# Optimization experiments

Hardware: AMD Instinct MI355X
Metric: run time of the kernel (lower is better)

Reference implementation:

```python
import jax, jax.numpy as jnp
import numpy as np

B, TC, TT, E, V = 512, 64, 16, 512, 256
E2 = E // 2


def entmax15(z):
    # exact sort-based 1.5-entmax over last axis (Peters et al., 2019)
    z = z / 2.0
    z = z - jnp.max(z, axis=-1, keepdims=True)  # shift-invariant, for stability
    z_srt = -jnp.sort(-z, axis=-1)
    d = z.shape[-1]
    rho = jnp.arange(1, d + 1, dtype=z.dtype)
    mean = jnp.cumsum(z_srt, axis=-1) / rho
    mean_sq = jnp.cumsum(z_srt * z_srt, axis=-1) / rho
    ss = rho * (mean_sq - mean * mean)
    delta = (1.0 - ss) / rho
    pos = delta > 0
    sqrt_d = jnp.where(pos, jnp.sqrt(jnp.where(pos, delta, 1.0)), 0.0)
    tau = mean - sqrt_d
    k = jnp.sum((tau <= z_srt).astype(jnp.int32), axis=-1, keepdims=True)
    tau_star = jnp.take_along_axis(tau, k - 1, axis=-1)
    y = jnp.clip(z - tau_star, 0.0)
    return y * y


def _mha(q_seq, kv, wq, wk, wv, bq, bk, bv, wo, bo):
    # single-head attention; q_seq: (T,B,E) decoder states, kv: (B,S,E) encoder memory
    e = q_seq.shape[-1]
    q = (q_seq @ wq.T + bq) * (1.0 / jnp.sqrt(jnp.asarray(e, q_seq.dtype)))
    k = kv @ wk.T + bk
    v = kv @ wv.T + bv
    a = jax.nn.softmax(jnp.einsum('tbe,bse->bts', q, k), axis=-1)
    o = jnp.einsum('bts,bse->tbe', a, v)
    return o @ wo.T + bo


def setup_inputs() -> dict:
    key = jax.random.key(0)
    ks = jax.random.split(key, 20)
    rn = lambda k, s, sc=1.0: sc * jax.random.normal(k, s, dtype=jnp.float32)
    z = lambda s: jnp.zeros(s, jnp.float32)
    return {
        'char_encoding': rn(ks[0], (B, TC, E)),
        'char_hn0': rn(ks[1], (B, E2)),
        'char_cn0': rn(ks[2], (B, E2)),
        'tag_encoding': rn(ks[3], (B, TT, E)),
        'tag_hn0': rn(ks[4], (B, E2)),
        'tag_cn0': rn(ks[5], (B, E2)),
        'true_output_seq': jax.random.uniform(ks[6], (B, TC, V), dtype=jnp.float32),
        'w_ih': rn(ks[7], (4 * E, V), 0.05),
        'w_hh': rn(ks[8], (4 * E, E), 0.05),
        'b_ih': z((4 * E,)),
        'b_hh': z((4 * E,)),
        'char_wq': rn(ks[9], (E, E), 0.05), 'char_wk': rn(ks[10], (E, E), 0.05), 'char_wv': rn(ks[11], (E, E), 0.05),
        'char_bq': z((E,)), 'char_bk': z((E,)), 'char_bv': z((E,)),
        'char_wo': rn(ks[12], (E, E), 0.05), 'char_bo': z((E,)),
        'tag_wq': rn(ks[13], (E, E), 0.05), 'tag_wk': rn(ks[14], (E, E), 0.05), 'tag_wv': rn(ks[15], (E, E), 0.05),
        'tag_bq': z((E,)), 'tag_bk': z((E,)), 'tag_bv': z((E,)),
        'tag_wo': rn(ks[16], (E, E), 0.05), 'tag_bo': z((E,)),
        'out_w': rn(ks[17], (V, 2 * E), 0.05),
        'out_b': z((V,)),
    }


def reference(char_encoding, char_hn0, char_cn0, tag_encoding, tag_hn0, tag_cn0, true_output_seq, w_ih, w_hh, b_ih, b_hh, char_wq, char_wk, char_wv, char_bq, char_bk, char_bv, char_wo, char_bo, tag_wq, tag_wk, tag_wv, tag_bq, tag_bk, tag_bv, tag_wo, tag_bo, out_w, out_b):
    # initial cell state = concat of the two encoders' final (h, c)
    h0 = jnp.concatenate([char_hn0, tag_hn0], axis=-1)
    c0 = jnp.concatenate([char_cn0, tag_cn0], axis=-1)
    # teacher forcing: input at t=0 is zeros, then true_output_seq[:, t]
    xs = jnp.concatenate([jnp.zeros_like(true_output_seq[:, :1]), true_output_seq[:, 1:]], axis=1)
    xs = jnp.swapaxes(xs, 0, 1)  # (T, B, V)

    def cell(carry, x):
        h, c = carry
        gates = x @ w_ih.T + b_ih + h @ w_hh.T + b_hh
        i, f, g, o = jnp.split(gates, 4, axis=-1)  # torch gate order i,f,g,o
        c = jax.nn.sigmoid(f) * c + jax.nn.sigmoid(i) * jnp.tanh(g)
        h = jax.nn.sigmoid(o) * jnp.tanh(c)
        return (h, c), h

    _, hs = jax.lax.scan(cell, (h0, c0), xs)  # (T, B, E)
    # attention queries only depend on per-step h, so batch all T queries at once
    ca = _mha(hs, char_encoding, char_wq, char_wk, char_wv, char_bq, char_bk, char_bv, char_wo, char_bo)
    ta = _mha(hs, tag_encoding, tag_wq, tag_wk, tag_wv, tag_bq, tag_bk, tag_bv, tag_wo, tag_bo)
    logits = jnp.concatenate([ca, ta], axis=-1) @ out_w.T + out_b  # (T, B, V)
    return jnp.swapaxes(entmax15(logits), 0, 1)  # (B, T, V)
```

## Files before the change

### kernel.cpp

```cpp
#include <hip/hip_runtime.h>

typedef unsigned short us;
typedef unsigned int u32;
typedef unsigned long long u64;
typedef __bf16 bf16x8 __attribute__((ext_vector_type(8)));
typedef float f32x4 __attribute__((ext_vector_type(4)));

#define MFMA(a,b,c) __builtin_amdgcn_mfma_f32_16x16x32_bf16(a,b,c,0,0,0)

__device__ __forceinline__ us f2bf(float f){
  u32 u = __builtin_bit_cast(u32, f);
  u += 0x7fffu + ((u>>16)&1u);
  return (us)(u>>16);
}
__device__ __forceinline__ float bf2f(us h){
  u32 u = ((u32)h)<<16;
  return __builtin_bit_cast(float, u);
}
__device__ __forceinline__ float sigf(float x){ return 1.0f/(1.0f+__expf(-x)); }
__device__ __forceinline__ float tanh_(float x){ float e=__expf(2.0f*x); return 1.0f - 2.0f/(e+1.0f); }


__global__ void k_prep_wperm(const float* __restrict__ w_hh, const float* __restrict__ w_ih,
                             const float* __restrict__ b_ih, const float* __restrict__ b_hh,
                             us* __restrict__ Wp, float* __restrict__ biasc){
  int n = blockIdx.x; int c = threadIdx.x;
  float v = (c < 512) ? w_hh[(size_t)n*512 + c] : w_ih[(size_t)n*256 + (c-512)];
  int g = n >> 9, eg = n & 511, eb = eg >> 4, ln = eg & 15;
  int kc = c >> 5, qd = (c >> 3) & 3, i = c & 7;
  size_t dst = ((((size_t)eb*24 + kc)*4 + g)*64 + (size_t)(qd*16 + ln))*8 + i;
  Wp[dst] = f2bf(v);
  if (c == 0) biasc[n] = b_ih[n] + b_hh[n];
}

__global__ void k_prep_state(const float* __restrict__ ch, const float* __restrict__ th,
                             const float* __restrict__ cc, const float* __restrict__ tc,
                             us* __restrict__ h0, float* __restrict__ c0){
  int i = blockIdx.x*256 + threadIdx.x;
  int b = i>>9, e = i&511;
  float hv = (e<256)? ch[b*256+e] : th[b*256+e-256];
  float cv = (e<256)? cc[b*256+e] : tc[b*256+e-256];
  h0[i] = f2bf(hv); c0[i] = cv;
}

__global__ void k_xprep(const float* __restrict__ x, us* __restrict__ xbf){
  int g = blockIdx.x*256 + threadIdx.x;
  int v0 = (g & 31) * 8;
  int b  = (g >> 5) & 511;
  int t  = g >> 14;
  const float4* src = (const float4*)(x + ((size_t)(b*64 + t))*256 + v0);
  float4 f0 = src[0], f1 = src[1];
  uint4 pk;
  pk.x = (u32)f2bf(f0.x) | ((u32)f2bf(f0.y)<<16);
  pk.y = (u32)f2bf(f0.z) | ((u32)f2bf(f0.w)<<16);
  pk.z = (u32)f2bf(f1.x) | ((u32)f2bf(f1.y)<<16);
  pk.w = (u32)f2bf(f1.z) | ((u32)f2bf(f1.w)<<16);
  *(uint4*)(xbf + ((size_t)t*512 + b)*256 + v0) = pk;
}

__global__ void k_uvec(const float* __restrict__ bq, const float* __restrict__ wk,
                       float* __restrict__ u){
  int j = blockIdx.x*128 + threadIdx.x;
  float a = 0.f;
  for (int e=0;e<512;++e) a += bq[e]*wk[(size_t)e*512 + j];
  u[j] = a;
}

__global__ void k_pvec(const float* __restrict__ wo, const float* __restrict__ bv,
                       const float* __restrict__ bo, float* __restrict__ p){
  int i = blockIdx.x*128 + threadIdx.x;
  float a = bo[i];
  for (int j=0;j<512;++j) a += wo[(size_t)i*512+j]*bv[j];
  p[i] = a;
}

__global__ void k_bc(const float* __restrict__ out_w, const float* __restrict__ pc,
                     const float* __restrict__ pt, const float* __restrict__ out_b,
                     float* __restrict__ bc){
  int v = threadIdx.x;
  float a = out_b[v];
  for (int i=0;i<512;++i) a += out_w[(size_t)v*1024+i]*pc[i];
  for (int i=0;i<512;++i) a += out_w[(size_t)v*1024+512+i]*pt[i];
  bc[v] = a;
}

template<bool TA, int OMODE>
__global__ __launch_bounds__(256) void k_pgemm(const float* __restrict__ A, int lda,
    const float* __restrict__ B, int ldb, void* C1, void* C2, int ldc, int K){
  __shared__ us As[64][40];
  __shared__ us Bs[64][40];
  int tid=threadIdx.x, w=tid>>6, lane=tid&63, qd=lane>>4, ln=lane&15;
  int m0 = blockIdx.x*64, n0 = blockIdx.y*64;
  f32x4 acc[4] = {};
  for (int kc=0; kc<K/32; ++kc){
    int k0 = kc*32;
    if (!TA){
      int r=tid>>2, c=(tid&3)*8;
      const float* ap = A + (size_t)(m0+r)*lda + k0 + c;
      float4 f0=*(const float4*)ap, f1=*(const float4*)(ap+4);
      uint4 pk;
      pk.x=(u32)f2bf(f0.x)|((u32)f2bf(f0.y)<<16);
      pk.y=(u32)f2bf(f0.z)|((u32)f2bf(f0.w)<<16);
      pk.z=(u32)f2bf(f1.x)|((u32)f2bf(f1.y)<<16);
      pk.w=(u32)f2bf(f1.z)|((u32)f2bf(f1.w)<<16);
      *(uint4*)&As[r][c] = pk;
    } else {
      int kk=tid>>3, mp=(tid&7)*8;
      const float* ap = A + (size_t)(k0+kk)*lda + m0 + mp;
      #pragma unroll
      for (int i=0;i<8;++i) As[mp+i][kk] = f2bf(ap[i]);
    }
    { int kk=tid>>3, np=(tid&7)*8;
      const float* bp = B + (size_t)(k0+kk)*ldb + n0 + np;
      #pragma unroll
      for (int i=0;i<8;++i) Bs[np+i][kk] = f2bf(bp[i]);
    }
    __syncthreads();
    bf16x8 a = *(const bf16x8*)&As[16*w+ln][qd*8];
    #pragma unroll
    for (int j=0;j<4;++j){
      bf16x8 bb = *(const bf16x8*)&Bs[16*j+ln][qd*8];
      acc[j] = MFMA(a, bb, acc[j]);
    }
    __syncthreads();
  }
  #pragma unroll
  for (int j=0;j<4;++j){
    #pragma unroll
    for (int r=0;r<4;++r){
      size_t idx = (size_t)(m0+16*w+qd*4+r)*ldc + (n0+16*j+ln);
      float v = acc[j][r];
      if (OMODE==0) ((float*)C1)[idx] = v;
      else if (OMODE==1) ((us*)C1)[idx] = f2bf(v);
      else {
        us h = f2bf(v);
        ((us*)C1)[idx] = h;
        ((us*)C2)[idx] = f2bf(v - bf2f(h));
      }
    }
  }
}

__global__ __launch_bounds__(256, 1) void k_lstm_all(
    const us* __restrict__ h0, const us* __restrict__ xbf,
    const us* __restrict__ Wp, const float* __restrict__ biasc,
    const float* __restrict__ c0, us* __restrict__ hs,
    unsigned* __restrict__ bars){
  extern __shared__ us Wf[];
  int tid = threadIdx.x, w = tid>>6, lane = tid&63, qd = lane>>4, ln = lane&15;
  int bb = blockIdx.x & 7, eb = blockIdx.x >> 3;
  int b0 = bb*64, e0 = eb*16;
  {
    const uint4* src = (const uint4*)(Wp + (size_t)eb*49152);
    uint4* dst = (uint4*)Wf;
    #pragma unroll
    for (int i=0;i<24;++i) dst[tid + 256*i] = src[tid + 256*i];
  }
  int bA = b0 + 16*w + ln;
  int bC = b0 + 16*w + qd*4;
  int e  = e0 + ln;
  float bias_[4], c_[4];
  #pragma unroll
  for (int j=0;j<4;++j) bias_[j] = biasc[j*512 + e];
  #pragma unroll
  for (int r=0;r<4;++r) c_[r] = c0[(size_t)(bC+r)*512 + e];
  __syncthreads();
  unsigned* bar = bars + bb*64;
  f32x4 xacc[4] = {};
  for (int t=0; t<64; ++t){
    if (t > 0){
      unsigned tgt = 32u*(unsigned)t;
      while (__hip_atomic_load(bar, __ATOMIC_RELAXED, __HIP_MEMORY_SCOPE_AGENT) < tgt)
        __builtin_amdgcn_s_sleep(1);
    }
    bf16x8 afr[16];
    if (t == 0){
      const us* hrow = h0 + (size_t)bA*512;
      #pragma unroll
      for (int kc=0; kc<16; ++kc)
        afr[kc] = *(const bf16x8*)(hrow + kc*32 + qd*8);
    } else {
      const u64* hq = (const u64*)(hs + ((size_t)bA*64 + (t-1))*512);
      u64 q0[16], q1[16];
      #pragma unroll
      for (int kc=0; kc<16; ++kc){
        q0[kc] = __hip_atomic_load(hq + kc*8 + qd*2 + 0, __ATOMIC_RELAXED, __HIP_MEMORY_SCOPE_AGENT);
        q1[kc] = __hip_atomic_load(hq + kc*8 + qd*2 + 1, __ATOMIC_RELAXED, __HIP_MEMORY_SCOPE_AGENT);
      }
      #pragma unroll
      for (int kc=0; kc<16; ++kc){
        union { u64 q[2]; bf16x8 v; } u_;
        u_.q[0] = q0[kc]; u_.q[1] = q1[kc];
        afr[kc] = u_.v;
      }
    }
    f32x4 acc[4] = {xacc[0], xacc[1], xacc[2], xacc[3]};
    #pragma unroll
    for (int kc=0; kc<16; ++kc){
      #pragma unroll
      for (int j=0;j<4;++j){
        bf16x8 bfrag = *(const bf16x8*)&Wf[(size_t)((kc*4+j)*64 + lane)*8];
        acc[j] = MFMA(afr[kc], bfrag, acc[j]);
      }
    }
    us hb[4];
    #pragma unroll
    for (int r=0;r<4;++r){
      float iv = acc[0][r]+bias_[0], fv = acc[1][r]+bias_[1];
      float gv = acc[2][r]+bias_[2], ov = acc[3][r]+bias_[3];
      float cc2 = sigf(fv)*c_[r] + sigf(iv)*tanh_(gv);
      c_[r] = cc2;
      hb[r] = f2bf(sigf(ov)*tanh_(cc2));
    }
    #pragma unroll
    for (int r=0;r<4;++r){
      u32 v = hb[r];
      u32 p = v | (((u32)__shfl_xor((int)v, 1)) << 16);
      u64 q = (u64)p | (((u64)(u32)__shfl_xor((int)p, 2)) << 32);
      if ((lane & 3) == 0){
        size_t idx = ((size_t)(bC+r)*64 + t)*512 + e0 + ln;
        __hip_atomic_store((u64*)(hs + idx), q, __ATOMIC_RELAXED, __HIP_MEMORY_SCOPE_AGENT);
      }
    }
    if (t < 63){
      __syncthreads();
      if (tid == 0)
        __hip_atomic_fetch_add(bar, 1u, __ATOMIC_RELAXED, __HIP_MEMORY_SCOPE_AGENT);
      const us* xrow = xbf + ((size_t)(t+1)*512 + bA)*256;
      f32x4 xa[4] = {};
      #pragma unroll
      for (int kx=0; kx<8; ++kx){
        bf16x8 xf = *(const bf16x8*)(xrow + kx*32 + qd*8);
        #pragma unroll
        for (int j=0;j<4;++j){
          bf16x8 bfrag = *(const bf16x8*)&Wf[(size_t)(((16+kx)*4+j)*64 + lane)*8];
          xa[j] = MFMA(xf, bfrag, xa[j]);
        }
      }
      #pragma unroll
      for (int j=0;j<4;++j) xacc[j] = xa[j];
    }
  }
}

__global__ __launch_bounds__(256) void k_gemm(
    const us* __restrict__ Ap, const us* __restrict__ W,
    const float* __restrict__ bias, float alpha, us* __restrict__ C){
  __shared__ us As[128][40];
  __shared__ us Ws[128][40];
  int tid = threadIdx.x; int w = tid>>6; int lane=tid&63;
  int qd=lane>>4, ln=lane&15;
  int m0 = blockIdx.x*128, n0 = blockIdx.y*128;
  int wm = (w&1)*64, wn=(w>>1)*64;
  f32x4 acc[4][4] = {};
  int row = tid>>1; int cp = (tid&1)*16;
  for (int kc=0;kc<16;++kc){
    int k0=kc*32;
    { const uint4* ap = (const uint4*)(Ap + (size_t)(m0+row)*512 + k0+cp);
      *(uint4*)&As[row][cp]=ap[0]; *(uint4*)&As[row][cp+8]=ap[1];
    }
    { const uint4* wp = (const uint4*)(W + (size_t)(n0+row)*512 + k0+cp);
      *(uint4*)&Ws[row][cp]=wp[0]; *(uint4*)&Ws[row][cp+8]=wp[1];
    }
    __syncthreads();
    bf16x8 af[4], bfr[4];
    #pragma unroll
    for (int i=0;i<4;++i) af[i]  = *(const bf16x8*)&As[wm+16*i+ln][qd*8];
    #pragma unroll
    for (int j=0;j<4;++j) bfr[j] = *(const bf16x8*)&Ws[wn+16*j+ln][qd*8];
    #pragma unroll
    for (int i=0;i<4;++i)
      #pragma unroll
      for (int j=0;j<4;++j) acc[i][j]=MFMA(af[i],bfr[j],acc[i][j]);
    __syncthreads();
  }
  #pragma unroll
  for (int j=0;j<4;++j){
    int col = n0+wn+16*j+ln;
    float bv = bias[col];
    #pragma unroll
    for (int i=0;i<4;++i){
      #pragma unroll
      for (int r=0;r<4;++r){
        int rm = m0+wm+16*i+qd*4+r;
        C[(size_t)rm*512 + col] = f2bf(alpha*(acc[i][j][r]+bv));
      }
    }
  }
}

template<int S>
struct alignas(16) ASmem3 {
  static constexpr int SP  = (S<32)?32:S;
  static constexpr int SPp = SP+8;
  us Pbh[64][SPp];
  us Pbl[64][SPp];
  union {
    us Es[S][72];
    struct { us Eh[64][72]; us El[64][72]; } t;
  } u;
  us Ph[64][72];
  us Pl[64][72];
};

template<int S, bool ACC>
__global__ __launch_bounds__(256) void k_attn3(const us* __restrict__ hGp,
    const float* __restrict__ enc, const us* __restrict__ Mvh,
    const us* __restrict__ Mvl, float* __restrict__ out){
  constexpr int NJ  = S/16;
  constexpr int KC2 = ((S<32)?32:S)/32;
  extern __shared__ char smraw[];
  ASmem3<S>& sm = *reinterpret_cast<ASmem3<S>*>(smraw);
  int b = blockIdx.x;
  int tid=threadIdx.x, w=tid>>6, lane=tid&63, qd=lane>>4, ln=lane&15;

  f32x4 sacc[NJ];
  #pragma unroll
  for (int j=0;j<NJ;++j) sacc[j] = (f32x4){0.f,0.f,0.f,0.f};
  const us* hrow = hGp + ((size_t)(b*64 + 16*w + ln))*512;
  for (int ec=0; ec<8; ++ec){
    int e0 = ec*64;
    { int s = tid>>2, ep=(tid&3)*16;
      if (S==64 || tid < 4*S){
        const float* ap = enc + ((size_t)b*S + s)*512 + e0 + ep;
        float4 f0=*(const float4*)ap, f1=*(const float4*)(ap+4);
        float4 f2=*(const float4*)(ap+8), f3=*(const float4*)(ap+12);
        float fv[16]={f0.x,f0.y,f0.z,f0.w,f1.x,f1.y,f1.z,f1.w,
                      f2.x,f2.y,f2.z,f2.w,f3.x,f3.y,f3.z,f3.w};
        u32 pk[8];
        #pragma unroll
        for (int i=0;i<8;++i)
          pk[i] = (u32)f2bf(fv[2*i]) | ((u32)f2bf(fv[2*i+1])<<16);
        uint4* d = (uint4*)&sm.u.Es[s][ep];
        d[0] = make_uint4(pk[0],pk[1],pk[2],pk[3]);
        d[1] = make_uint4(pk[4],pk[5],pk[6],pk[7]);
      }
    }
    __syncthreads();
    #pragma unroll
    for (int kcl=0;kcl<2;++kcl){
      bf16x8 a = *(const bf16x8*)(hrow + e0 + kcl*32 + qd*8);
      #pragma unroll
      for (int j=0;j<NJ;++j){
        bf16x8 bb = *(const bf16x8*)&sm.u.Es[16*j+ln][kcl*32+qd*8];
        sacc[j] = MFMA(a, bb, sacc[j]);
      }
    }
    __syncthreads();
  }

  #pragma unroll
  for (int r=0;r<4;++r){
    float m = sacc[0][r];
    #pragma unroll
    for (int j=1;j<NJ;++j) m = fmaxf(m, sacc[j][r]);
    #pragma unroll
    for (int dl=1; dl<16; dl<<=1) m = fmaxf(m, __shfl_xor(m, dl));
    float ssum = 0.f;
    #pragma unroll
    for (int j=0;j<NJ;++j){ float e_=__expf(sacc[j][r]-m); sacc[j][r]=e_; ssum+=e_; }
    #pragma unroll
    for (int dl=1; dl<16; dl<<=1) ssum += __shfl_xor(ssum, dl);
    float inv = 1.0f/ssum;
    int R = 16*w + qd*4 + r;
    #pragma unroll
    for (int j=0;j<NJ;++j){
      float pv = sacc[j][r]*inv;
      us h = f2bf(pv);
      sm.Pbh[R][16*j+ln] = h;
      sm.Pbl[R][16*j+ln] = f2bf(pv - bf2f(h));
    }
    if (S==16){ sm.Pbh[R][16+ln]=0; sm.Pbl[R][16+ln]=0; }
  }

  f32x4 Lacc[4][4] = {};
  for (int ec=0; ec<8; ++ec){
    int e0 = ec*64;
    { int s = tid>>2, ep=(tid&3)*16;
      if (S==64 || tid < 4*S){
        const float* ap = enc + ((size_t)b*S + s)*512 + e0 + ep;
        float4 f0=*(const float4*)ap, f1=*(const float4*)(ap+4);
        float4 f2=*(const float4*)(ap+8), f3=*(const float4*)(ap+12);
        float fv[16]={f0.x,f0.y,f0.z,f0.w,f1.x,f1.y,f1.z,f1.w,
                      f2.x,f2.y,f2.z,f2.w,f3.x,f3.y,f3.z,f3.w};
        #pragma unroll
        for (int i=0;i<16;++i){
          float v = fv[i]; us h = f2bf(v);
          sm.u.t.Eh[ep+i][s] = h;
          sm.u.t.El[ep+i][s] = f2bf(v - bf2f(h));
        }
      } else if (S==16 && tid < 128){
        int s2 = 16 + ((tid-64)>>2);
        #pragma unroll
        for (int i=0;i<16;++i){ sm.u.t.Eh[ep+i][s2]=0; sm.u.t.El[ep+i][s2]=0; }
      }
    }
    __syncthreads();
    f32x4 pacc[4] = {};
    #pragma unroll
    for (int kcl=0;kcl<KC2;++kcl){
      bf16x8 ah = *(const bf16x8*)&sm.Pbh[16*w+ln][kcl*32+qd*8];
      bf16x8 al = *(const bf16x8*)&sm.Pbl[16*w+ln][kcl*32+qd*8];
      #pragma unroll
      for (int j=0;j<4;++j){
        bf16x8 bh = *(const bf16x8*)&sm.u.t.Eh[16*j+ln][kcl*32+qd*8];
        bf16x8 bl = *(const bf16x8*)&sm.u.t.El[16*j+ln][kcl*32+qd*8];
        pacc[j] = MFMA(ah, bh, pacc[j]);
        pacc[j] = MFMA(ah, bl, pacc[j]);
        pacc[j] = MFMA(al, bh, pacc[j]);
      }
    }
    #pragma unroll
    for (int j=0;j<4;++j)
      #pragma unroll
      for (int r=0;r<4;++r){
        float v = pacc[j][r]; us h = f2bf(v);
        sm.Ph[16*w+qd*4+r][16*j+ln] = h;
        sm.Pl[16*w+qd*4+r][16*j+ln] = f2bf(v - bf2f(h));
      }
    __syncthreads();
    #pragma unroll
    for (int kcl=0;kcl<2;++kcl){
      bf16x8 ah[4], al[4];
      #pragma unroll
      for (int i=0;i<4;++i){
        ah[i] = *(const bf16x8*)&sm.Ph[16*i+ln][kcl*32+qd*8];
        al[i] = *(const bf16x8*)&sm.Pl[16*i+ln][kcl*32+qd*8];
      }
      #pragma unroll
      for (int j=0;j<4;++j){
        int v = 64*w + 16*j + ln;
        bf16x8 mh = *(const bf16x8*)(Mvh + (size_t)v*512 + e0 + kcl*32 + qd*8);
        bf16x8 ml = *(const bf16x8*)(Mvl + (size_t)v*512 + e0 + kcl*32 + qd*8);
        #pragma unroll
        for (int i=0;i<4;++i){
          Lacc[i][j] = MFMA(ah[i], mh, Lacc[i][j]);
          Lacc[i][j] = MFMA(ah[i], ml, Lacc[i][j]);
          Lacc[i][j] = MFMA(al[i], mh, Lacc[i][j]);
        }
      }
    }
  }
  #pragma unroll
  for (int i=0;i<4;++i){
    #pragma unroll
    for (int j=0;j<4;++j){
      int v = 64*w + 16*j + ln;
      #pragma unroll
      for (int r=0;r<4;++r){
        size_t addr = ((size_t)b*64 + 16*i + qd*4 + r)*256 + v;
        if (ACC) out[addr] += Lacc[i][j][r];
        else     out[addr]  = Lacc[i][j][r];
      }
    }
  }
}

__global__ __launch_bounds__(256) void k_entmax(float* __restrict__ out,
                                                const float* __restrict__ bc){
  int tid=threadIdx.x; int w=tid>>6; int lane=tid&63;
  float4 bcv = *(const float4*)(bc + lane*4);
  int base = blockIdx.x*16 + w*4;
  for (int i=0;i<4;++i){
    int row = base + i;
    float* rp = out + (size_t)row*256 + lane*4;
    float4 d = *(const float4*)rp;
    float z[4] = {0.5f*(d.x+bcv.x), 0.5f*(d.y+bcv.y), 0.5f*(d.z+bcv.z), 0.5f*(d.w+bcv.w)};
    float m = fmaxf(fmaxf(z[0],z[1]), fmaxf(z[2],z[3]));
    #pragma unroll
    for (int dl=1; dl<64; dl<<=1) m = fmaxf(m, __shfl_xor(m, dl));
    #pragma unroll
    for (int k=0;k<4;++k) z[k] -= m;
    float tau = -1.0f;
    for (int it=0; it<14; ++it){
      float s1=0.f, s2=0.f;
      #pragma unroll
      for (int k=0;k<4;++k){
        float dd = z[k]-tau; dd = fmaxf(dd, 0.f);
        s1 += dd; s2 += dd*dd;
      }
      #pragma unroll
      for (int dl=1; dl<64; dl<<=1){ s1 += __shfl_xor(s1, dl); s2 += __shfl_xor(s2, dl); }
      tau += (s2 - 1.0f) / (2.0f*fmaxf(s1, 1e-12f));
    }
    float4 y;
    { float dd;
      dd = fmaxf(z[0]-tau,0.f); y.x = dd*dd;
      dd = fmaxf(z[1]-tau,0.f); y.y = dd*dd;
      dd = fmaxf(z[2]-tau,0.f); y.z = dd*dd;
      dd = fmaxf(z[3]-tau,0.f); y.w = dd*dd;
    }
    *(float4*)rp = y;
  }
}


extern "C" void kernel_launch(void* const* d_in, const int* in_sizes, int n_in,
                              void* d_out, int out_size, void* d_ws, size_t ws_size,
                              hipStream_t stream){
  (void)in_sizes; (void)n_in; (void)out_size; (void)ws_size;
  const float* char_enc = (const float*)d_in[0];
  const float* char_hn0 = (const float*)d_in[1];
  const float* char_cn0 = (const float*)d_in[2];
  const float* tag_enc  = (const float*)d_in[3];
  const float* tag_hn0  = (const float*)d_in[4];
  const float* tag_cn0  = (const float*)d_in[5];
  const float* true_out = (const float*)d_in[6];
  const float* w_ih = (const float*)d_in[7];
  const float* w_hh = (const float*)d_in[8];
  const float* b_ih = (const float*)d_in[9];
  const float* b_hh = (const float*)d_in[10];
  const float* c_wq = (const float*)d_in[11];
  const float* c_wk = (const float*)d_in[12];
  const float* c_wv = (const float*)d_in[13];
  const float* c_bq = (const float*)d_in[14];
  const float* c_bv = (const float*)d_in[16];
  const float* c_wo = (const float*)d_in[17];
  const float* c_bo = (const float*)d_in[18];
  const float* t_wq = (const float*)d_in[19];
  const float* t_wk = (const float*)d_in[20];
  const float* t_wv = (const float*)d_in[21];
  const float* t_bq = (const float*)d_in[22];
  const float* t_bv = (const float*)d_in[24];
  const float* t_wo = (const float*)d_in[25];
  const float* t_bo = (const float*)d_in[26];
  const float* out_w = (const float*)d_in[27];
  const float* out_b = (const float*)d_in[28];
  float* out = (float*)d_out;

  char* base = (char*)d_ws;
  char* regA = base;
  us*    Wp    = (us*)   (regA + 0);
  float* biasc = (float*)(regA + 3145728);
  us*    h0    = (us*)   (regA + 3153920);
  float* cst   = (float*)(regA + 3678208);
  float* M1f   = (float*)(regA + 4726784);
  float* M2f   = (float*)(regA + 5251072);
  us*    xbf   = (us*)   (regA + 5775360);
  us*    hG    = (us*)   regA;
  char* regB = base + 33554432;
  us*    Gc_w  = (us*)(regB + 0);
  us*    Gt_w  = (us*)(regB + 524288);
  us*    M1vh  = (us*)(regB + 1048576);
  us*    M1vl  = (us*)(regB + 1310720);
  us*    M2vh  = (us*)(regB + 1572864);
  us*    M2vl  = (us*)(regB + 1835008);
  float* u_c   = (float*)(regB + 2097152);
  float* u_t   = (float*)(regB + 2099200);
  float* p_c   = (float*)(regB + 2101248);
  float* p_t   = (float*)(regB + 2103296);
  float* bc    = (float*)(regB + 2105344);
  us*    hs    = (us*)(base + 33554432 + 2106368);
  unsigned* bars = (unsigned*)(base + 33554432 + 2106368 + 33554432);

  static bool attr_done = false;
  if (!attr_done){
    hipFuncSetAttribute(reinterpret_cast<const void*>(&k_lstm_all),
                        hipFuncAttributeMaxDynamicSharedMemorySize, 131072);
    attr_done = true;
  }

  hipMemsetAsync(bars, 0, 2048, stream);
  k_prep_wperm<<<2048, 768, 0, stream>>>(w_hh, w_ih, b_ih, b_hh, Wp, biasc);
  k_prep_state<<<1024, 256, 0, stream>>>(char_hn0, tag_hn0, char_cn0, tag_cn0, h0, cst);
  k_xprep<<<4096, 256, 0, stream>>>(true_out, xbf);
  k_pgemm<true,1><<<dim3(8,8),256,0,stream>>>(c_wk, 512, c_wq, 512, Gc_w, nullptr, 512, 512);
  k_pgemm<true,1><<<dim3(8,8),256,0,stream>>>(t_wk, 512, t_wq, 512, Gt_w, nullptr, 512, 512);
  k_pgemm<false,0><<<dim3(4,8),256,0,stream>>>(out_w,     1024, c_wo, 512, M1f, nullptr, 512, 512);
  k_pgemm<false,0><<<dim3(4,8),256,0,stream>>>(out_w+512, 1024, t_wo, 512, M2f, nullptr, 512, 512);
  k_pgemm<false,2><<<dim3(4,8),256,0,stream>>>(M1f, 512, c_wv, 512, M1vh, M1vl, 512, 512);
  k_pgemm<false,2><<<dim3(4,8),256,0,stream>>>(M2f, 512, t_wv, 512, M2vh, M2vl, 512, 512);
  k_uvec<<<4,128,0,stream>>>(c_bq, c_wk, u_c);
  k_uvec<<<4,128,0,stream>>>(t_bq, t_wk, u_t);
  k_pvec<<<4,128,0,stream>>>(c_wo, c_bv, c_bo, p_c);
  k_pvec<<<4,128,0,stream>>>(t_wo, t_bv, t_bo, p_t);
  k_bc<<<1,256,0,stream>>>(out_w, p_c, p_t, out_b, bc);

  k_lstm_all<<<256, 256, 98304, stream>>>(h0, xbf, Wp, biasc, cst, hs, bars);

  const float scale = 0.044194173824159216f;
  k_gemm<<<dim3(256,4),256,0,stream>>>(hs, Gc_w, u_c, scale, hG);
  k_attn3<64,false><<<512,256,sizeof(ASmem3<64>),stream>>>(hG, char_enc, M1vh, M1vl, out);
  k_gemm<<<dim3(256,4),256,0,stream>>>(hs, Gt_w, u_t, scale, hG);
  k_attn3<16,true ><<<512,256,sizeof(ASmem3<16>),stream>>>(hG, tag_enc, M2vh, M2vl, out);
  k_entmax<<<2048,256,0,stream>>>(out, bc);
}
```

Before: 1.117 ms.

## Split LSTM recurrence K-dimension across wave pairs and double the block count

The persistent LSTM kernel now runs 512 blocks of 32 batch rows instead of 256 blocks of 64. Within each block, pairs of waves split the hidden-state reduction in half and combine their partial gate sums through a swizzled shared-memory exchange. The input-weight slice is no longer held in LDS and is read from global memory, which cuts shared memory so two blocks fit per CU. The aim is to shorten the per-step serial critical path by using more CUs and smaller per-wave MFMA chains, at the cost of an extra __syncthreads per step, more barrier participants per group, and global-memory weight reads.

```diff
diff --git a/kernel.cpp b/kernel.cpp
--- a/kernel.cpp
+++ b/kernel.cpp
@@ -141,82 +141,110 @@
   }
 }
 
-__global__ __launch_bounds__(256, 1) void k_lstm_all(
+__global__ __launch_bounds__(256, 2) void k_lstm_all2(
     const us* __restrict__ h0, const us* __restrict__ xbf,
     const us* __restrict__ Wp, const float* __restrict__ biasc,
     const float* __restrict__ c0, us* __restrict__ hs,
     unsigned* __restrict__ bars){
-  extern __shared__ us Wf[];
+  extern __shared__ us smem[];
+  us*    Wf   = smem;
+  float* exch = (float*)(smem + 32768);
   int tid = threadIdx.x, w = tid>>6, lane = tid&63, qd = lane>>4, ln = lane&15;
-  int bb = blockIdx.x & 7, eb = blockIdx.x >> 3;
-  int b0 = bb*64, e0 = eb*16;
+  int hf = w & 1, p = w >> 1;
+  int bb = blockIdx.x & 15, eb = blockIdx.x >> 4;
+  int b0 = bb*32, e0 = eb*16;
   {
     const uint4* src = (const uint4*)(Wp + (size_t)eb*49152);
     uint4* dst = (uint4*)Wf;
     #pragma unroll
-    for (int i=0;i<24;++i) dst[tid + 256*i] = src[tid + 256*i];
-  }
-  int bA = b0 + 16*w + ln;
-  int bC = b0 + 16*w + qd*4;
+    for (int i=0;i<16;++i) dst[tid + 256*i] = src[tid + 256*i];
+  }
+  int bA = b0 + 16*p + ln;
+  int bC = b0 + 16*p + qd*4 + hf*2;
   int e  = e0 + ln;
-  float bias_[4], c_[4];
+  float bias_[4];
   #pragma unroll
   for (int j=0;j<4;++j) bias_[j] = biasc[j*512 + e];
+  float c_[2];
   #pragma unroll
-  for (int r=0;r<4;++r) c_[r] = c0[(size_t)(bC+r)*512 + e];
+  for (int r=0;r<2;++r) c_[r] = c0[(size_t)(bC+r)*512 + e];
   __syncthreads();
   unsigned* bar = bars + bb*64;
-  f32x4 xacc[4] = {};
+  f32x4 xa[4] = {};
+  const int kh0 = hf*8;
   for (int t=0; t<64; ++t){
     if (t > 0){
       unsigned tgt = 32u*(unsigned)t;
       while (__hip_atomic_load(bar, __ATOMIC_RELAXED, __HIP_MEMORY_SCOPE_AGENT) < tgt)
-        __builtin_amdgcn_s_sleep(1);
-    }
-    bf16x8 afr[16];
+        __builtin_amdgcn_s_sleep(2);
+    }
+    bf16x8 afr[8];
     if (t == 0){
       const us* hrow = h0 + (size_t)bA*512;
       #pragma unroll
-      for (int kc=0; kc<16; ++kc)
-        afr[kc] = *(const bf16x8*)(hrow + kc*32 + qd*8);
+      for (int k=0;k<8;++k)
+        afr[k] = *(const bf16x8*)(hrow + (kh0+k)*32 + qd*8);
     } else {
       const u64* hq = (const u64*)(hs + ((size_t)bA*64 + (t-1))*512);
-      u64 q0[16], q1[16];
-      #pragma unroll
-      for (int kc=0; kc<16; ++kc){
-        q0[kc] = __hip_atomic_load(hq + kc*8 + qd*2 + 0, __ATOMIC_RELAXED, __HIP_MEMORY_SCOPE_AGENT);
-        q1[kc] = __hip_atomic_load(hq + kc*8 + qd*2 + 1, __ATOMIC_RELAXED, __HIP_MEMORY_SCOPE_AGENT);
-      }
-      #pragma unroll
-      for (int kc=0; kc<16; ++kc){
+      u64 q0[8], q1[8];
+      #pragma unroll
+      for (int k=0;k<8;++k){
+        q0[k] = __hip_atomic_load(hq + (kh0+k)*8 + qd*2 + 0, __ATOMIC_RELAXED, __HIP_MEMORY_SCOPE_AGENT);
+        q1[k] = __hip_atomic_load(hq + (kh0+k)*8 + qd*2 + 1, __ATOMIC_RELAXED, __HIP_MEMORY_SCOPE_AGENT);
+      }
+      #pragma unroll
+      for (int k=0;k<8;++k){
         union { u64 q[2]; bf16x8 v; } u_;
-        u_.q[0] = q0[kc]; u_.q[1] = q1[kc];
-        afr[kc] = u_.v;
-      }
-    }
-    f32x4 acc[4] = {xacc[0], xacc[1], xacc[2], xacc[3]};
-    #pragma unroll
-    for (int kc=0; kc<16; ++kc){
+        u_.q[0] = q0[k]; u_.q[1] = q1[k];
+        afr[k] = u_.v;
+      }
+    }
+    f32x4 acc[4] = {xa[0], xa[1], xa[2], xa[3]};
+    #pragma unroll
+    for (int k=0;k<8;++k){
+      int kc = kh0 + k;
       #pragma unroll
       for (int j=0;j<4;++j){
         bf16x8 bfrag = *(const bf16x8*)&Wf[(size_t)((kc*4+j)*64 + lane)*8];
-        acc[j] = MFMA(afr[kc], bfrag, acc[j]);
-      }
-    }
-    us hb[4];
-    #pragma unroll
-    for (int r=0;r<4;++r){
-      float iv = acc[0][r]+bias_[0], fv = acc[1][r]+bias_[1];
-      float gv = acc[2][r]+bias_[2], ov = acc[3][r]+bias_[3];
+        acc[j] = MFMA(afr[k], bfrag, acc[j]);
+      }
+    }
+    {
+      int rw = (hf^1)*2;
+      #pragma unroll
+      for (int k=0;k<2;++k){
+        int c = lane*2 + k;
+        int cs = c ^ ((c>>3)&7);
+        float4 v = { acc[2*k+0][rw], acc[2*k+0][rw+1],
+                     acc[2*k+1][rw], acc[2*k+1][rw+1] };
+        *(float4*)(exch + (size_t)w*512 + cs*4) = v;
+      }
+      __syncthreads();
+      #pragma unroll
+      for (int k=0;k<2;++k){
+        int c = lane*2 + k;
+        int cs = c ^ ((c>>3)&7);
+        float4 v = *(const float4*)(exch + (size_t)(w^1)*512 + cs*4);
+        acc[2*k+0][hf*2+0] += v.x;
+        acc[2*k+0][hf*2+1] += v.y;
+        acc[2*k+1][hf*2+0] += v.z;
+        acc[2*k+1][hf*2+1] += v.w;
+      }
+    }
+    us hb[2];
+    #pragma unroll
+    for (int r=0;r<2;++r){
+      float iv = acc[0][hf*2+r]+bias_[0], fv = acc[1][hf*2+r]+bias_[1];
+      float gv = acc[2][hf*2+r]+bias_[2], ov = acc[3][hf*2+r]+bias_[3];
       float cc2 = sigf(fv)*c_[r] + sigf(iv)*tanh_(gv);
       c_[r] = cc2;
       hb[r] = f2bf(sigf(ov)*tanh_(cc2));
     }
     #pragma unroll
-    for (int r=0;r<4;++r){
+    for (int r=0;r<2;++r){
       u32 v = hb[r];
-      u32 p = v | (((u32)__shfl_xor((int)v, 1)) << 16);
-      u64 q = (u64)p | (((u64)(u32)__shfl_xor((int)p, 2)) << 32);
+      u32 pk = v | (((u32)__shfl_xor((int)v, 1)) << 16);
+      u64 q = (u64)pk | (((u64)(u32)__shfl_xor((int)pk, 2)) << 32);
       if ((lane & 3) == 0){
         size_t idx = ((size_t)(bC+r)*64 + t)*512 + e0 + ln;
         __hip_atomic_store((u64*)(hs + idx), q, __ATOMIC_RELAXED, __HIP_MEMORY_SCOPE_AGENT);
@@ -227,18 +255,19 @@
       if (tid == 0)
         __hip_atomic_fetch_add(bar, 1u, __ATOMIC_RELAXED, __HIP_MEMORY_SCOPE_AGENT);
       const us* xrow = xbf + ((size_t)(t+1)*512 + bA)*256;
-      f32x4 xa[4] = {};
-      #pragma unroll
-      for (int kx=0; kx<8; ++kx){
+      f32x4 xn[4] = {};
+      #pragma unroll
+      for (int k=0;k<4;++k){
+        int kx = hf*4 + k;
         bf16x8 xf = *(const bf16x8*)(xrow + kx*32 + qd*8);
         #pragma unroll
         for (int j=0;j<4;++j){
-          bf16x8 bfrag = *(const bf16x8*)&Wf[(size_t)(((16+kx)*4+j)*64 + lane)*8];
-          xa[j] = MFMA(xf, bfrag, xa[j]);
+          bf16x8 bw = *(const bf16x8*)(Wp + ((size_t)(eb*24 + 16 + kx)*4 + j)*512 + lane*8);
+          xn[j] = MFMA(xf, bw, xn[j]);
         }
       }
       #pragma unroll
-      for (int j=0;j<4;++j) xacc[j] = xa[j];
+      for (int j=0;j<4;++j) xa[j] = xn[j];
     }
   }
 }
@@ -555,12 +584,12 @@
 
   static bool attr_done = false;
   if (!attr_done){
-    hipFuncSetAttribute(reinterpret_cast<const void*>(&k_lstm_all),
-                        hipFuncAttributeMaxDynamicSharedMemorySize, 131072);
+    hipFuncSetAttribute(reinterpret_cast<const void*>(&k_lstm_all2),
+                        hipFuncAttributeMaxDynamicSharedMemorySize, 73728);
     attr_done = true;
   }
 
-  hipMemsetAsync(bars, 0, 2048, stream);
+  hipMemsetAsync(bars, 0, 4096, stream);
   k_prep_wperm<<<2048, 768, 0, stream>>>(w_hh, w_ih, b_ih, b_hh, Wp, biasc);
   k_prep_state<<<1024, 256, 0, stream>>>(char_hn0, tag_hn0, char_cn0, tag_cn0, h0, cst);
   k_xprep<<<4096, 256, 0, stream>>>(true_out, xbf);
@@ -576,7 +605,7 @@
   k_pvec<<<4,128,0,stream>>>(t_wo, t_bv, t_bo, p_t);
   k_bc<<<1,256,0,stream>>>(out_w, p_c, p_t, out_b, bc);
 
-  k_lstm_all<<<256, 256, 98304, stream>>>(h0, xbf, Wp, biasc, cst, hs, bars);
+  k_lstm_all2<<<512, 256, 73728, stream>>>(h0, xbf, Wp, biasc, cst, hs, bars);
 
   const float scale = 0.044194173824159216f;
   k_gemm<<<dim3(256,4),256,0,stream>>>(hs, Gc_w, u_c, scale, hG);
```

Result: slower. 1.265 ms (+13.3%).
